# Optimization experiments

Measured on AMD Instinct MI355X. Metric: run time of the kernel, lower is better.

## Reference

```python
import jax, jax.numpy as jnp
import numpy as np

PATCH = 4   # patch_size
TOPK = 2    # top_k

B, H, W, C = 4, 128, 128, 256
FF, E = 1024, 4


def setup_inputs() -> dict:
    key = jax.random.key(0)
    k1, k2, k3, k4 = jax.random.split(key, 4)
    x = jax.random.normal(k1, (B, H, W, C), dtype=jnp.float32)
    Wg = jax.random.normal(k2, (E, C), dtype=jnp.float32) * 0.01   # router gate (std=0.01 init)
    lim1 = (6.0 / (C + FF)) ** 0.5                                  # xavier_uniform bounds
    W1 = jax.random.uniform(k3, (E, FF, C), minval=-lim1, maxval=lim1, dtype=jnp.float32)
    b1 = jnp.zeros((E, FF), dtype=jnp.float32)
    W2 = jax.random.uniform(k4, (E, C, FF), minval=-lim1, maxval=lim1, dtype=jnp.float32)
    b2 = jnp.zeros((E, C), dtype=jnp.float32)
    return {"x": x, "Wg": Wg, "W1": W1, "b1": b1, "W2": W2, "b2": b2}


def reference(x, Wg, W1, b1, W2, b2):
    Bs, Hs, Ws, Cs = x.shape
    Es = Wg.shape[0]
    ph = pw = PATCH
    nh, nw = Hs // ph, Ws // pw
    P = nh * nw
    # [B, nh, ph, nw, pw, C]
    xp = x.reshape(Bs, nh, ph, nw, pw, Cs)
    # --- router: per-patch avg pool + linear gate ---
    means = xp.mean(axis=(2, 4))                                  # [B, nh, nw, C]
    logits = jnp.einsum('bhwc,ec->bhwe', means, Wg).reshape(Bs, P, Es)
    probs = jax.nn.softmax(logits, axis=-1)
    w, idx = jax.lax.top_k(probs, TOPK)                           # [B, P, K]
    w = w / (w.sum(axis=-1, keepdims=True) + 1e-9)
    # dense combine weights per expert: [B, P, E]
    comb = (jax.nn.one_hot(idx, Es, dtype=w.dtype) * w[..., None]).sum(axis=-2)
    # --- expert dispatch/combine over patch tokens ---
    tokens = xp.transpose(0, 1, 3, 2, 4, 5).reshape(Bs, P, ph * pw, Cs)  # [B,P,T,C]
    out = jnp.zeros_like(tokens)
    for e in range(Es):  # small fixed expert set
        h = jax.nn.gelu(jnp.einsum('bptc,fc->bptf', tokens, W1[e]) + b1[e],
                        approximate=False)
        y = jnp.einsum('bptf,cf->bptc', h, W2[e]) + b2[e]
        out = out + comb[:, :, e, None, None] * y
    # reassemble patches -> [B, H, W, C]
    out = out.reshape(Bs, nh, nw, ph, pw, Cs).transpose(0, 1, 3, 2, 4, 5)
    return out.reshape(Bs, Hs, Ws, Cs)
```

## Files before the change

### kernel.cpp

```cpp
#include <hip/hip_runtime.h>
#include <hip/hip_bf16.h>
#include <cstdint>

#define NB 4
#define NH 128
#define NW 128
#define NC 256
#define NFF 1024
#define NE 4
#define NPATCH 4096
#define PPB 4
#define BM 64
#define FFC 128
#define NCHUNK (NFF / FFC)

typedef __attribute__((ext_vector_type(8))) short short8;
typedef __attribute__((ext_vector_type(8))) unsigned short ushort8;
typedef __attribute__((ext_vector_type(4))) float f32x4;

__device__ __forceinline__ unsigned short f2b(float f) {
  union { float f; uint32_t u; } v; v.f = f;
  uint32_t u = v.u + 0x7FFFu + ((v.u >> 16) & 1u);
  return (unsigned short)(u >> 16);
}

__device__ __forceinline__ float gelu_f(float v) {
  float u = v * v;
  float t = __builtin_fmaf(u, 0.044715f, 1.0f) * v;
  float e = __builtin_amdgcn_exp2f(t * -2.3022083f);
  return v * __builtin_amdgcn_rcpf(1.0f + e);
}

__device__ __forceinline__ void bar_lgkm() {
  asm volatile("s_waitcnt lgkmcnt(0)" ::: "memory");
  __builtin_amdgcn_s_barrier();
}

__global__ __launch_bounds__(256) void convert_kernel(
    const float* __restrict__ W1, const float* __restrict__ W2,
    unsigned short* __restrict__ W1b, unsigned short* __restrict__ W2b, int n) {
  int i = blockIdx.x * blockDim.x + threadIdx.x;
  if (i < n) {
    W1b[i] = f2b(W1[i]);
    W2b[i] = f2b(W2[i]);
  }
}

__global__ __launch_bounds__(256) void router_kernel(
    const float* __restrict__ x, const float* __restrict__ Wg,
    int* __restrict__ cnt, int* __restrict__ plist, float* __restrict__ wlist) {
  int p = blockIdx.x;
  int b = p >> 10, pi = p & 1023;
  int phi = pi >> 5, pwi = pi & 31;
  int c = threadIdx.x;

  const float* base = x + (((size_t)(b * NH + phi * 4) * NW) + pwi * 4) * NC + c;
  float s = 0.f;
#pragma unroll
  for (int i = 0; i < 4; i++)
#pragma unroll
    for (int j = 0; j < 4; j++)
      s += base[(i * NW + j) * NC];
  float mean = s * (1.f / 16.f);

  __shared__ float m_lds[NC];
  __shared__ double logit_lds[NE];
  m_lds[c] = mean;
  __syncthreads();

  int wid = c >> 6, lane = c & 63;
  {
    const float* wg = Wg + wid * NC;
    double acc = 0.0;
#pragma unroll
    for (int q = 0; q < 4; q++)
      acc += (double)m_lds[lane + q * 64] * (double)wg[lane + q * 64];
    for (int off = 32; off; off >>= 1) acc += __shfl_down(acc, off);
    if (lane == 0) logit_lds[wid] = acc;
  }
  __syncthreads();

  if (c == 0) {
    double l[NE], pp[NE];
    double mx = -1e300;
#pragma unroll
    for (int i = 0; i < NE; i++) { l[i] = logit_lds[i]; mx = fmax(mx, l[i]); }
    double sum = 0.0;
#pragma unroll
    for (int i = 0; i < NE; i++) { pp[i] = exp(l[i] - mx); sum += pp[i]; }
#pragma unroll
    for (int i = 0; i < NE; i++) pp[i] /= sum;
    int i1 = 0; double p1 = pp[0];
    for (int i = 1; i < NE; i++) if (pp[i] > p1) { p1 = pp[i]; i1 = i; }
    int i2 = -1; double p2 = -1.0;
    for (int i = 0; i < NE; i++) {
      if (i == i1) continue;
      if (pp[i] > p2) { p2 = pp[i]; i2 = i; }
    }
    double den = p1 + p2 + 1e-9;
    float w1 = (float)(p1 / den), w2 = (float)(p2 / den);
    int pos0 = atomicAdd(&cnt[0 * NE + i1], 1);
    plist[(0 * NE + i1) * NPATCH + pos0] = p;
    wlist[(0 * NE + i1) * NPATCH + pos0] = w1;
    int pos1 = atomicAdd(&cnt[1 * NE + i2], 1);
    plist[(1 * NE + i2) * NPATCH + pos1] = p;
    wlist[(1 * NE + i2) * NPATCH + pos1] = w2;
  }
}

__global__ __launch_bounds__(256, 3) void ffn_kernel(
    const float* __restrict__ x, const float* __restrict__ b1,
    const float* __restrict__ b2, const unsigned short* __restrict__ W1b,
    const unsigned short* __restrict__ W2b, const int* __restrict__ cnt,
    const int* __restrict__ plist, const float* __restrict__ wlist,
    float* __restrict__ out0, float* __restrict__ out1, int mode) {
  __shared__ unsigned short Xl[BM * NC];
  __shared__ unsigned short Hl[BM * FFC];

  int bid = blockIdx.x;
  int grp = bid & 7;
  int e = grp >> 1, slot = grp & 1;
  int tile = bid >> 3;
  int le = slot * NE + e;
  int n = cnt[le];
  if (tile * PPB >= n) return;

  int tid = threadIdx.x, lane = tid & 63, wid = tid >> 6;
  int l15 = lane & 15;
  int kgrp = (lane >> 4) * 8;

  const int*   pl = plist + le * NPATCH + tile * PPB;
  const float* wl = wlist + le * NPATCH + tile * PPB;

  {
    int r  = tid >> 2;
    int c0 = (tid & 3) * 64;
    int pid = (tile * PPB + wid < n) ? pl[wid] : -1;
    int t = r & 15;
    if (pid >= 0) {
      int b = pid >> 10, pi = pid & 1023;
      int phi = pi >> 5, pwi = pi & 31;
      const float* src =
          x + (((size_t)(b * NH + phi * 4 + (t >> 2)) * NW) + pwi * 4 + (t & 3)) * NC + c0;
#pragma unroll
      for (int q = 0; q < 8; q++) {
        float4 v0 = *reinterpret_cast<const float4*>(src + q * 8);
        float4 v1 = *reinterpret_cast<const float4*>(src + q * 8 + 4);
        ushort8 h;
        h[0] = f2b(v0.x); h[1] = f2b(v0.y); h[2] = f2b(v0.z); h[3] = f2b(v0.w);
        h[4] = f2b(v1.x); h[5] = f2b(v1.y); h[6] = f2b(v1.z); h[7] = f2b(v1.w);
        int boff = (r * 512 + (c0 + q * 8) * 2) ^ ((r & 7) << 4);
        *reinterpret_cast<ushort8*>((char*)Xl + boff) = h;
      }
    } else {
      ushort8 h = (ushort8)0;
#pragma unroll
      for (int q = 0; q < 8; q++) {
        int boff = (r * 512 + (c0 + q * 8) * 2) ^ ((r & 7) << 4);
        *reinterpret_cast<ushort8*>((char*)Xl + boff) = h;
      }
    }
  }
  bar_lgkm();

  f32x4 acc2[4][4];
#pragma unroll
  for (int a = 0; a < 4; a++)
#pragma unroll
    for (int b = 0; b < 4; b++)
#pragma unroll
      for (int j = 0; j < 4; j++) acc2[a][b][j] = 0.f;

  const unsigned short* W1e = W1b + (size_t)e * NFF * NC;
  const unsigned short* W2e = W2b + (size_t)e * NC * NFF;
  const float* b1e = b1 + e * NFF;
  const float* b2e = b2 + e * NC;

  for (int fc = 0; fc < NCHUNK; fc++) {
    f32x4 acc1[2][4];
#pragma unroll
    for (int a = 0; a < 2; a++)
#pragma unroll
      for (int b = 0; b < 4; b++)
#pragma unroll
        for (int j = 0; j < 4; j++) acc1[a][b][j] = 0.f;

#pragma unroll
    for (int ks = 0; ks < 8; ks++) {
      int k = ks * 32 + kgrp;
      short8 bX[4];
#pragma unroll
      for (int nt = 0; nt < 4; nt++) {
        int row = nt * 16 + l15;
        int boff = (row * 512 + k * 2) ^ ((row & 7) << 4);
        bX[nt] = *reinterpret_cast<const short8*>((const char*)Xl + boff);
      }
#pragma unroll
      for (int ftl = 0; ftl < 2; ftl++) {
        int f = fc * FFC + wid * 32 + ftl * 16 + l15;
        short8 aW = *reinterpret_cast<const short8*>(W1e + (size_t)f * NC + k);
#pragma unroll
        for (int nt = 0; nt < 4; nt++)
          acc1[ftl][nt] = __builtin_amdgcn_mfma_f32_16x16x32_bf16(aW, bX[nt], acc1[ftl][nt], 0, 0, 0);
      }
    }

    bar_lgkm();

#pragma unroll
    for (int ftl = 0; ftl < 2; ftl++) {
      int f0 = wid * 32 + ftl * 16 + (lane >> 4) * 4;
      float4 bv = *reinterpret_cast<const float4*>(b1e + fc * FFC + f0);
#pragma unroll
      for (int nt = 0; nt < 4; nt++) {
        int token = nt * 16 + l15;
        ushort4 hp;
        hp.x = f2b(gelu_f(acc1[ftl][nt][0] + bv.x));
        hp.y = f2b(gelu_f(acc1[ftl][nt][1] + bv.y));
        hp.z = f2b(gelu_f(acc1[ftl][nt][2] + bv.z));
        hp.w = f2b(gelu_f(acc1[ftl][nt][3] + bv.w));
        int boff = (token * 256 + f0 * 2) ^ ((token & 7) << 4);
        *reinterpret_cast<ushort4*>((char*)Hl + boff) = hp;
      }
    }
    bar_lgkm();

#pragma unroll
    for (int ks = 0; ks < 4; ks++) {
      int kf = ks * 32 + kgrp;
      short8 aH[4];
#pragma unroll
      for (int rt = 0; rt < 4; rt++) {
        int row = rt * 16 + l15;
        int boff = (row * 256 + kf * 2) ^ ((row & 7) << 4);
        aH[rt] = *reinterpret_cast<const short8*>((const char*)Hl + boff);
      }
#pragma unroll
      for (int ct = 0; ct < 4; ct++) {
        int c = wid * 64 + ct * 16 + l15;
        short8 bW = *reinterpret_cast<const short8*>(W2e + (size_t)c * NFF + fc * FFC + kf);
#pragma unroll
        for (int rt = 0; rt < 4; rt++)
          acc2[ct][rt] = __builtin_amdgcn_mfma_f32_16x16x32_bf16(aH[rt], bW, acc2[ct][rt], 0, 0, 0);
      }
    }
  }

  float* obase = (slot == 0) ? out0 : out1;
  float bias2[4];
#pragma unroll
  for (int ct = 0; ct < 4; ct++) bias2[ct] = b2e[wid * 64 + ct * 16 + l15];

#pragma unroll
  for (int rt = 0; rt < 4; rt++) {
    if (tile * PPB + rt >= n) continue;
    int pid = pl[rt];
    float wgt = wl[rt];
    int b = pid >> 10, pi = pid & 1023;
    int phi = pi >> 5, pwi = pi & 31;
#pragma unroll
    for (int i = 0; i < 4; i++) {
      int t = (lane >> 4) * 4 + i;
      float* dst =
          obase + (((size_t)(b * NH + phi * 4 + (t >> 2)) * NW) + pwi * 4 + (t & 3)) * NC;
#pragma unroll
      for (int ct = 0; ct < 4; ct++) {
        int c = wid * 64 + ct * 16 + l15;
        float val = wgt * (acc2[ct][rt][i] + bias2[ct]);
        if (mode == 0) dst[c] = val;
        else atomicAdd(&dst[c], val);
      }
    }
  }
}

__global__ __launch_bounds__(256) void combine_kernel(
    float* __restrict__ out, const float* __restrict__ y1, int n4) {
  int i = blockIdx.x * blockDim.x + threadIdx.x;
  int stride = gridDim.x * blockDim.x;
  for (; i < n4; i += stride) {
    float4 a = reinterpret_cast<float4*>(out)[i];
    float4 b = reinterpret_cast<const float4*>(y1)[i];
    a.x += b.x; a.y += b.y; a.z += b.z; a.w += b.w;
    reinterpret_cast<float4*>(out)[i] = a;
  }
}

extern "C" void kernel_launch(void* const* d_in, const int* in_sizes, int n_in,
                              void* d_out, int out_size, void* d_ws, size_t ws_size,
                              hipStream_t stream) {
  const float* x  = (const float*)d_in[0];
  const float* Wg = (const float*)d_in[1];
  const float* W1 = (const float*)d_in[2];
  const float* b1 = (const float*)d_in[3];
  const float* W2 = (const float*)d_in[4];
  const float* b2 = (const float*)d_in[5];
  float* out = (float*)d_out;

  char* ws = (char*)d_ws;
  unsigned short* W1b = (unsigned short*)ws;
  unsigned short* W2b = (unsigned short*)(ws + (size_t)2 * 1024 * 1024);
  int*   cnt   = (int*)(ws + (size_t)4 * 1024 * 1024);
  int*   plist = (int*)(ws + (size_t)4 * 1024 * 1024 + 256);
  float* wlist = (float*)(ws + (size_t)4 * 1024 * 1024 + 256 +
                          (size_t)2 * NE * NPATCH * sizeof(int));
  float* y1buf = (float*)(ws + (size_t)8 * 1024 * 1024);

  size_t need = (size_t)8 * 1024 * 1024 + (size_t)NB * NH * NW * NC * sizeof(float);
  int mode = (ws_size >= need) ? 0 : 1;

  hipMemsetAsync(cnt, 0, 2 * NE * sizeof(int), stream);
  if (mode == 1)
    hipMemsetAsync(out, 0, (size_t)out_size * sizeof(float), stream);

  convert_kernel<<<dim3(4096), dim3(256), 0, stream>>>(W1, W2, W1b, W2b, NE * NFF * NC);
  router_kernel<<<dim3(NPATCH), dim3(256), 0, stream>>>(x, Wg, cnt, plist, wlist);

  float* out1 = (mode == 0) ? y1buf : out;
  ffn_kernel<<<dim3(8192), dim3(256), 0, stream>>>(
      x, b1, b2, W1b, W2b, cnt, plist, wlist, out, out1, mode);

  if (mode == 0) {
    int n4 = NB * NH * NW * NC / 4;
    combine_kernel<<<dim3(2048), dim3(256), 0, stream>>>(out, y1buf, n4);
  }
}
```

Measured before the change: 466.0 us.

## Route patches by expert pair and fuse both experts into one FFN block

The router now groups each patch by its ordered (top1, top2) expert pair. One FFN block runs both experts for its four patches, with the routing weights folded into the GELU output, so the two partial results add up inside the same accumulator. This removes the second output buffer, the combine kernel, the memset launches and the duplicate x loads and stores. The FF chunk grows to 256, and the next chunk's GEMM1 and GELU are overlapped with the previous chunk's GEMM2 through register staging. In exchange it uses more registers (occupancy hint lowered to 2), launches a 16-pair grid that can leave tiles partly empty, and weights the hidden activation before bf16 rounding, which changes precision slightly.

```diff
diff --git a/kernel.cpp b/kernel.cpp
--- a/kernel.cpp
+++ b/kernel.cpp
@@ -9,10 +9,10 @@
 #define NFF 1024
 #define NE 4
 #define NPATCH 4096
+#define NPAIR 16
 #define PPB 4
 #define BM 64
-#define FFC 128
-#define NCHUNK (NFF / FFC)
+#define FFC 256
 
 typedef __attribute__((ext_vector_type(8))) short short8;
 typedef __attribute__((ext_vector_type(8))) unsigned short ushort8;
@@ -38,8 +38,10 @@
 
 __global__ __launch_bounds__(256) void convert_kernel(
     const float* __restrict__ W1, const float* __restrict__ W2,
-    unsigned short* __restrict__ W1b, unsigned short* __restrict__ W2b, int n) {
+    unsigned short* __restrict__ W1b, unsigned short* __restrict__ W2b,
+    int* __restrict__ cnt, int n) {
   int i = blockIdx.x * blockDim.x + threadIdx.x;
+  if (i < NPAIR) cnt[i] = 0;
   if (i < n) {
     W1b[i] = f2b(W1[i]);
     W2b[i] = f2b(W2[i]);
@@ -48,7 +50,7 @@
 
 __global__ __launch_bounds__(256) void router_kernel(
     const float* __restrict__ x, const float* __restrict__ Wg,
-    int* __restrict__ cnt, int* __restrict__ plist, float* __restrict__ wlist) {
+    int* __restrict__ cnt, int* __restrict__ plist, float2* __restrict__ wlist) {
   int p = blockIdx.x;
   int b = p >> 10, pi = p & 1023;
   int phi = pi >> 5, pwi = pi & 31;
@@ -99,43 +101,48 @@
     }
     double den = p1 + p2 + 1e-9;
     float w1 = (float)(p1 / den), w2 = (float)(p2 / den);
-    int pos0 = atomicAdd(&cnt[0 * NE + i1], 1);
-    plist[(0 * NE + i1) * NPATCH + pos0] = p;
-    wlist[(0 * NE + i1) * NPATCH + pos0] = w1;
-    int pos1 = atomicAdd(&cnt[1 * NE + i2], 1);
-    plist[(1 * NE + i2) * NPATCH + pos1] = p;
-    wlist[(1 * NE + i2) * NPATCH + pos1] = w2;
-  }
-}
-
-__global__ __launch_bounds__(256, 3) void ffn_kernel(
+    int pr = i1 * NE + i2;
+    int pos = atomicAdd(&cnt[pr], 1);
+    plist[pr * NPATCH + pos] = p;
+    wlist[pr * NPATCH + pos] = make_float2(w1, w2);
+  }
+}
+
+__global__ __launch_bounds__(256, 2) void ffn_kernel(
     const float* __restrict__ x, const float* __restrict__ b1,
     const float* __restrict__ b2, const unsigned short* __restrict__ W1b,
     const unsigned short* __restrict__ W2b, const int* __restrict__ cnt,
-    const int* __restrict__ plist, const float* __restrict__ wlist,
-    float* __restrict__ out0, float* __restrict__ out1, int mode) {
+    const int* __restrict__ plist, const float2* __restrict__ wlist,
+    float* __restrict__ out) {
   __shared__ unsigned short Xl[BM * NC];
   __shared__ unsigned short Hl[BM * FFC];
 
   int bid = blockIdx.x;
-  int grp = bid & 7;
-  int e = grp >> 1, slot = grp & 1;
-  int tile = bid >> 3;
-  int le = slot * NE + e;
-  int n = cnt[le];
-  if (tile * PPB >= n) return;
+  int pr = bid & 15;
+  int e1 = pr >> 2, e2 = pr & 3;
+  int tile = bid >> 4;
+  int n = cnt[pr];
+  int pbase = tile * PPB;
+  if (pbase >= n) return;
 
   int tid = threadIdx.x, lane = tid & 63, wid = tid >> 6;
   int l15 = lane & 15;
   int kgrp = (lane >> 4) * 8;
 
-  const int*   pl = plist + le * NPATCH + tile * PPB;
-  const float* wl = wlist + le * NPATCH + tile * PPB;
+  const int*    pl = plist + pr * NPATCH + pbase;
+  const float2* wl = wlist + pr * NPATCH + pbase;
+
+  float wvA[PPB], wvB[PPB];
+#pragma unroll
+  for (int q = 0; q < PPB; q++) {
+    if (pbase + q < n) { float2 w = wl[q]; wvA[q] = w.x; wvB[q] = w.y; }
+    else { wvA[q] = 0.f; wvB[q] = 0.f; }
+  }
 
   {
     int r  = tid >> 2;
     int c0 = (tid & 3) * 64;
-    int pid = (tile * PPB + wid < n) ? pl[wid] : -1;
+    int pid = (pbase + (r >> 4) < n) ? pl[r >> 4] : -1;
     int t = r & 15;
     if (pid >= 0) {
       int b = pid >> 10, pi = pid & 1023;
@@ -163,6 +170,13 @@
   }
   bar_lgkm();
 
+  const unsigned short* W1A = W1b + (size_t)e1 * NFF * NC;
+  const unsigned short* W1B = W1b + (size_t)e2 * NFF * NC;
+  const unsigned short* W2A = W2b + (size_t)e1 * NC * NFF;
+  const unsigned short* W2B = W2b + (size_t)e2 * NC * NFF;
+  const float* b1A = b1 + e1 * NFF;
+  const float* b1B = b1 + e2 * NFF;
+
   f32x4 acc2[4][4];
 #pragma unroll
   for (int a = 0; a < 4; a++)
@@ -171,20 +185,16 @@
 #pragma unroll
       for (int j = 0; j < 4; j++) acc2[a][b][j] = 0.f;
 
-  const unsigned short* W1e = W1b + (size_t)e * NFF * NC;
-  const unsigned short* W2e = W2b + (size_t)e * NC * NFF;
-  const float* b1e = b1 + e * NFF;
-  const float* b2e = b2 + e * NC;
-
-  for (int fc = 0; fc < NCHUNK; fc++) {
-    f32x4 acc1[2][4];
-#pragma unroll
-    for (int a = 0; a < 2; a++)
+  f32x4 acc1[4][4];
+  ushort4 hreg[16];
+
+  auto GEMM1 = [&](const unsigned short* W1e, int fc) {
+#pragma unroll
+    for (int a = 0; a < 4; a++)
 #pragma unroll
       for (int b = 0; b < 4; b++)
 #pragma unroll
         for (int j = 0; j < 4; j++) acc1[a][b][j] = 0.f;
-
 #pragma unroll
     for (int ks = 0; ks < 8; ks++) {
       int k = ks * 32 + kgrp;
@@ -196,49 +206,100 @@
         bX[nt] = *reinterpret_cast<const short8*>((const char*)Xl + boff);
       }
 #pragma unroll
-      for (int ftl = 0; ftl < 2; ftl++) {
-        int f = fc * FFC + wid * 32 + ftl * 16 + l15;
+      for (int ftl = 0; ftl < 4; ftl++) {
+        int f = fc * FFC + wid * 64 + ftl * 16 + l15;
         short8 aW = *reinterpret_cast<const short8*>(W1e + (size_t)f * NC + k);
 #pragma unroll
         for (int nt = 0; nt < 4; nt++)
           acc1[ftl][nt] = __builtin_amdgcn_mfma_f32_16x16x32_bf16(aW, bX[nt], acc1[ftl][nt], 0, 0, 0);
       }
     }
-
+  };
+
+  auto FUSED = [&](const unsigned short* W2p, int fcp,
+                   const float* b1e, int fc, bool sideB, bool domfma) {
+#pragma unroll
+    for (int ks = 0; ks < 8; ks++) {
+      if (domfma) {
+        int kf = ks * 32 + kgrp;
+        short8 aH[4];
+#pragma unroll
+        for (int rt = 0; rt < 4; rt++) {
+          int row = rt * 16 + l15;
+          int boff = (row * 512 + kf * 2) ^ ((row & 7) << 4);
+          aH[rt] = *reinterpret_cast<const short8*>((const char*)Hl + boff);
+        }
+#pragma unroll
+        for (int ct = 0; ct < 4; ct++) {
+          int c = wid * 64 + ct * 16 + l15;
+          short8 bW = *reinterpret_cast<const short8*>(W2p + (size_t)c * NFF + fcp * FFC + kf);
+#pragma unroll
+          for (int rt = 0; rt < 4; rt++)
+            acc2[ct][rt] = __builtin_amdgcn_mfma_f32_16x16x32_bf16(aH[rt], bW, acc2[ct][rt], 0, 0, 0);
+        }
+      }
+#pragma unroll
+      for (int j = 0; j < 2; j++) {
+        int g = ks * 2 + j;
+        int ftl = g >> 2, nt = g & 3;
+        int f0 = wid * 64 + ftl * 16 + (lane >> 4) * 4;
+        float4 bv = *reinterpret_cast<const float4*>(b1e + fc * FFC + f0);
+        float w = sideB ? wvB[nt] : wvA[nt];
+        ushort4 hp;
+        hp.x = f2b(gelu_f(acc1[ftl][nt][0] + bv.x) * w);
+        hp.y = f2b(gelu_f(acc1[ftl][nt][1] + bv.y) * w);
+        hp.z = f2b(gelu_f(acc1[ftl][nt][2] + bv.z) * w);
+        hp.w = f2b(gelu_f(acc1[ftl][nt][3] + bv.w) * w);
+        hreg[g] = hp;
+      }
+    }
+  };
+
+  auto WRITEH = [&]() {
+#pragma unroll
+    for (int g = 0; g < 16; g++) {
+      int ftl = g >> 2, nt = g & 3;
+      int token = nt * 16 + l15;
+      int f0 = wid * 64 + ftl * 16 + (lane >> 4) * 4;
+      int boff = (token * 512 + f0 * 2) ^ ((token & 7) << 4);
+      *reinterpret_cast<ushort4*>((char*)Hl + boff) = hreg[g];
+    }
+  };
+
+  GEMM1(W1A, 0);
+  FUSED(nullptr, 0, b1A, 0, false, false);
+  WRITEH();
+  bar_lgkm();
+
+#pragma unroll 1
+  for (int i = 1; i < 8; i++) {
+    bool sB = (i >= 4);
+    int fc = i & 3, fcp = (i - 1) & 3;
+    const unsigned short* W1e = sB ? W1B : W1A;
+    const float* b1e = sB ? b1B : b1A;
+    const unsigned short* W2p = (i - 1 >= 4) ? W2B : W2A;
+    GEMM1(W1e, fc);
+    FUSED(W2p, fcp, b1e, fc, sB, true);
     bar_lgkm();
-
-#pragma unroll
-    for (int ftl = 0; ftl < 2; ftl++) {
-      int f0 = wid * 32 + ftl * 16 + (lane >> 4) * 4;
-      float4 bv = *reinterpret_cast<const float4*>(b1e + fc * FFC + f0);
-#pragma unroll
-      for (int nt = 0; nt < 4; nt++) {
-        int token = nt * 16 + l15;
-        ushort4 hp;
-        hp.x = f2b(gelu_f(acc1[ftl][nt][0] + bv.x));
-        hp.y = f2b(gelu_f(acc1[ftl][nt][1] + bv.y));
-        hp.z = f2b(gelu_f(acc1[ftl][nt][2] + bv.z));
-        hp.w = f2b(gelu_f(acc1[ftl][nt][3] + bv.w));
-        int boff = (token * 256 + f0 * 2) ^ ((token & 7) << 4);
-        *reinterpret_cast<ushort4*>((char*)Hl + boff) = hp;
-      }
-    }
+    WRITEH();
     bar_lgkm();
-
-#pragma unroll
-    for (int ks = 0; ks < 4; ks++) {
+  }
+
+  {
+#pragma unroll
+    for (int ks = 0; ks < 8; ks++) {
       int kf = ks * 32 + kgrp;
       short8 aH[4];
 #pragma unroll
       for (int rt = 0; rt < 4; rt++) {
         int row = rt * 16 + l15;
-        int boff = (row * 256 + kf * 2) ^ ((row & 7) << 4);
+        int boff = (row * 512 + kf * 2) ^ ((row & 7) << 4);
         aH[rt] = *reinterpret_cast<const short8*>((const char*)Hl + boff);
       }
 #pragma unroll
       for (int ct = 0; ct < 4; ct++) {
         int c = wid * 64 + ct * 16 + l15;
-        short8 bW = *reinterpret_cast<const short8*>(W2e + (size_t)c * NFF + fc * FFC + kf);
+        short8 bW = *reinterpret_cast<const short8*>(W2B + (size_t)c * NFF + 3 * FFC + kf);
 #pragma unroll
         for (int rt = 0; rt < 4; rt++)
           acc2[ct][rt] = __builtin_amdgcn_mfma_f32_16x16x32_bf16(aH[rt], bW, acc2[ct][rt], 0, 0, 0);
@@ -246,43 +307,31 @@
     }
   }
 
-  float* obase = (slot == 0) ? out0 : out1;
-  float bias2[4];
-#pragma unroll
-  for (int ct = 0; ct < 4; ct++) bias2[ct] = b2e[wid * 64 + ct * 16 + l15];
-
+  float b2A4[4], b2B4[4];
+#pragma unroll
+  for (int ct = 0; ct < 4; ct++) {
+    int c = wid * 64 + ct * 16 + l15;
+    b2A4[ct] = b2[e1 * NC + c];
+    b2B4[ct] = b2[e2 * NC + c];
+  }
 #pragma unroll
   for (int rt = 0; rt < 4; rt++) {
-    if (tile * PPB + rt >= n) continue;
+    if (pbase + rt >= n) continue;
     int pid = pl[rt];
-    float wgt = wl[rt];
+    float wA = wvA[rt], wB = wvB[rt];
     int b = pid >> 10, pi = pid & 1023;
     int phi = pi >> 5, pwi = pi & 31;
 #pragma unroll
-    for (int i = 0; i < 4; i++) {
-      int t = (lane >> 4) * 4 + i;
+    for (int i2 = 0; i2 < 4; i2++) {
+      int t = (lane >> 4) * 4 + i2;
       float* dst =
-          obase + (((size_t)(b * NH + phi * 4 + (t >> 2)) * NW) + pwi * 4 + (t & 3)) * NC;
+          out + (((size_t)(b * NH + phi * 4 + (t >> 2)) * NW) + pwi * 4 + (t & 3)) * NC;
 #pragma unroll
       for (int ct = 0; ct < 4; ct++) {
         int c = wid * 64 + ct * 16 + l15;
-        float val = wgt * (acc2[ct][rt][i] + bias2[ct]);
-        if (mode == 0) dst[c] = val;
-        else atomicAdd(&dst[c], val);
-      }
-    }
-  }
-}
-
-__global__ __launch_bounds__(256) void combine_kernel(
-    float* __restrict__ out, const float* __restrict__ y1, int n4) {
-  int i = blockIdx.x * blockDim.x + threadIdx.x;
-  int stride = gridDim.x * blockDim.x;
-  for (; i < n4; i += stride) {
-    float4 a = reinterpret_cast<float4*>(out)[i];
-    float4 b = reinterpret_cast<const float4*>(y1)[i];
-    a.x += b.x; a.y += b.y; a.z += b.z; a.w += b.w;
-    reinterpret_cast<float4*>(out)[i] = a;
+        dst[c] = acc2[ct][rt][i2] + wA * b2A4[ct] + wB * b2B4[ct];
+      }
+    }
   }
 }
 
@@ -300,28 +349,14 @@
   char* ws = (char*)d_ws;
   unsigned short* W1b = (unsigned short*)ws;
   unsigned short* W2b = (unsigned short*)(ws + (size_t)2 * 1024 * 1024);
-  int*   cnt   = (int*)(ws + (size_t)4 * 1024 * 1024);
-  int*   plist = (int*)(ws + (size_t)4 * 1024 * 1024 + 256);
-  float* wlist = (float*)(ws + (size_t)4 * 1024 * 1024 + 256 +
-                          (size_t)2 * NE * NPATCH * sizeof(int));
-  float* y1buf = (float*)(ws + (size_t)8 * 1024 * 1024);
-
-  size_t need = (size_t)8 * 1024 * 1024 + (size_t)NB * NH * NW * NC * sizeof(float);
-  int mode = (ws_size >= need) ? 0 : 1;
-
-  hipMemsetAsync(cnt, 0, 2 * NE * sizeof(int), stream);
-  if (mode == 1)
-    hipMemsetAsync(out, 0, (size_t)out_size * sizeof(float), stream);
-
-  convert_kernel<<<dim3(4096), dim3(256), 0, stream>>>(W1, W2, W1b, W2b, NE * NFF * NC);
+  int*    cnt   = (int*)(ws + (size_t)4 * 1024 * 1024);
+  int*    plist = (int*)(ws + (size_t)4 * 1024 * 1024 + 256);
+  float2* wlist = (float2*)(ws + (size_t)4 * 1024 * 1024 + 256 +
+                            (size_t)NPAIR * NPATCH * sizeof(int));
+
+  convert_kernel<<<dim3(4096), dim3(256), 0, stream>>>(W1, W2, W1b, W2b, cnt, NE * NFF * NC);
   router_kernel<<<dim3(NPATCH), dim3(256), 0, stream>>>(x, Wg, cnt, plist, wlist);
 
-  float* out1 = (mode == 0) ? y1buf : out;
-  ffn_kernel<<<dim3(8192), dim3(256), 0, stream>>>(
-      x, b1, b2, W1b, W2b, cnt, plist, wlist, out, out1, mode);
-
-  if (mode == 0) {
-    int n4 = NB * NH * NW * NC / 4;
-    combine_kernel<<<dim3(2048), dim3(256), 0, stream>>>(out, y1buf, n4);
-  }
-}
+  ffn_kernel<<<dim3(NPAIR * (NPATCH / PPB)), dim3(256), 0, stream>>>(
+      x, b1, b2, W1b, W2b, cnt, plist, wlist, out);
+}
```

Measured after the change: 490.0 us. 5.1% more time.
